# Kernel tuning notes

Hardware: AMD Instinct MI355X
Metric: run time of the kernel (lower is better)

Reference implementation:

```python
import jax, jax.numpy as jnp
import numpy as np

EPS = 1e-5


def conv1x1(x, w, b=None):
    # x: [B,C,H,W], w: [O,C] (1x1 conv kernel squeezed)
    y = jnp.einsum('bchw,oc->bohw', x, w)
    if b is not None:
        y = y + b[None, :, None, None]
    return y


def bn_inf(x, g, b, m, v):
    scale = g / jnp.sqrt(v + EPS)
    return (x - m[None, :, None, None]) * scale[None, :, None, None] + b[None, :, None, None]


def setup_inputs() -> dict:
    B, C, H, W = 2, 256, 80, 80
    Ck, Cv, Co = 64, 128, 256
    key = jax.random.key(0)
    ks = jax.random.split(key, 16)
    d = {}
    d['x'] = jax.random.normal(ks[0], (B, C, H, W), dtype=jnp.float32)
    d['y'] = jax.random.normal(ks[1], (B, C, H, W), dtype=jnp.float32)
    s = 1.0 / np.sqrt(C)
    d['fk_w'] = jax.random.normal(ks[2], (Ck, C), dtype=jnp.float32) * s
    d['fk_g'] = jnp.ones((Ck,), jnp.float32)
    d['fk_b'] = jnp.zeros((Ck,), jnp.float32)
    d['fk_m'] = jax.random.normal(ks[3], (Ck,), dtype=jnp.float32) * 0.1
    d['fk_v'] = jax.random.uniform(ks[4], (Ck,), minval=0.5, maxval=1.5, dtype=jnp.float32)
    d['fq_w'] = jax.random.normal(ks[5], (Ck, C), dtype=jnp.float32) * s
    d['fq_g'] = jnp.ones((Ck,), jnp.float32)
    d['fq_b'] = jnp.zeros((Ck,), jnp.float32)
    d['fq_m'] = jax.random.normal(ks[6], (Ck,), dtype=jnp.float32) * 0.1
    d['fq_v'] = jax.random.uniform(ks[7], (Ck,), minval=0.5, maxval=1.5, dtype=jnp.float32)
    d['fv_w'] = jax.random.normal(ks[8], (Cv, C), dtype=jnp.float32) * s
    d['fv_b'] = jnp.zeros((Cv,), jnp.float32)
    d['W_w'] = jax.random.normal(ks[9], (Co, Cv), dtype=jnp.float32) * (1.0 / np.sqrt(Cv))
    d['W_b'] = jnp.zeros((Co,), jnp.float32)
    d['gamma'] = jnp.array([0.5], jnp.float32)
    return d


def reference(x, y, fk_w, fk_g, fk_b, fk_m, fk_v, fq_w, fq_g, fq_b, fq_m, fq_v, fv_w, fv_b, W_w, W_b, gamma):
    B, C, H, W = x.shape
    Ck = fk_w.shape[0]
    Cv = fv_w.shape[0]
    N = H * W
    # key from x, query/value from y (1x1 conv + BN projections)
    k = bn_inf(conv1x1(x, fk_w), fk_g, fk_b, fk_m, fk_v).reshape(B, Ck, N)          # [B,Ck,N]
    q = bn_inf(conv1x1(y, fq_w), fq_g, fq_b, fq_m, fq_v).reshape(B, Ck, N)          # [B,Ck,N]
    v = conv1x1(y, fv_w, fv_b).reshape(B, Cv, N)                                     # [B,Cv,N]
    sim = jnp.einsum('bkn,bkm->bnm', q, k) * (Ck ** -0.5)                            # [B,N,N]
    sim = jax.nn.softmax(sim, axis=-1)
    ctx = jnp.einsum('bnm,bvm->bvn', sim, v).reshape(B, Cv, H, W)                    # [B,Cv,H,W]
    ctx = conv1x1(ctx, W_w, W_b)                                                     # [B,Co,H,W]
    return gamma[0] * ctx + x
```

## Files before the change

kernel.cpp:

```cpp
#include <hip/hip_runtime.h>
#include <math.h>

#define NB   2
#define CIN  256
#define NN   6400
#define CKd  64
#define CVd  128
#define COd  256

using bf16   = __bf16;
using bf16x4 = __attribute__((ext_vector_type(4))) bf16;
using bf16x8 = __attribute__((ext_vector_type(8))) bf16;
using f32x4  = __attribute__((ext_vector_type(4))) float;

__device__ __forceinline__ void lds_cp16(const void* g, void* l) {
    __builtin_amdgcn_global_load_lds((const __attribute__((address_space(1))) void*)g,
                                     (__attribute__((address_space(3))) void*)l, 16, 0, 0);
}

__launch_bounds__(256)
__global__ void tcvt_prep_kernel(const float* __restrict__ x, const float* __restrict__ y,
                                 bf16* __restrict__ xT, bf16* __restrict__ yT,
                                 const float* __restrict__ fk_w, const float* __restrict__ fk_g,
                                 const float* __restrict__ fk_b, const float* __restrict__ fk_m,
                                 const float* __restrict__ fk_v,
                                 const float* __restrict__ fq_w, const float* __restrict__ fq_g,
                                 const float* __restrict__ fq_b, const float* __restrict__ fq_m,
                                 const float* __restrict__ fq_v,
                                 const float* __restrict__ fv_w, const float* __restrict__ fv_b,
                                 const float* __restrict__ W_w,  const float* __restrict__ W_b,
                                 bf16* __restrict__ wkb, bf16* __restrict__ wqb,
                                 bf16* __restrict__ wvb, bf16* __restrict__ wob,
                                 float* __restrict__ bias)
{
    __shared__ __align__(16) bf16 t_lds[64][68];

    if (blockIdx.z == 4) {
        const int idx = (blockIdx.y * 100 + blockIdx.x) * 256 + threadIdx.x;
        const float QS = 0.18033688011112042f;
        if (idx < 16384) {
            const int co = idx >> 8;
            const float a = fk_g[co] * rsqrtf(fk_v[co] + 1e-5f);
            wkb[idx] = (bf16)(fk_w[idx] * a);
        } else if (idx < 32768) {
            const int i = idx - 16384, co = i >> 8;
            const float a = fq_g[co] * rsqrtf(fq_v[co] + 1e-5f) * QS;
            wqb[i] = (bf16)(fq_w[i] * a);
        } else if (idx < 65536) {
            const int i = idx - 32768;
            wvb[i] = (bf16)fv_w[i];
        } else if (idx < 98304) {
            const int i = idx - 65536;
            wob[i] = (bf16)W_w[i];
        } else if (idx < 98816) {
            const int j = idx - 98304;
            if (j < 64)       { const float a = fk_g[j] * rsqrtf(fk_v[j] + 1e-5f); bias[j] = fk_b[j] - fk_m[j] * a; }
            else if (j < 128) { const int c = j - 64; const float a = fq_g[c] * rsqrtf(fq_v[c] + 1e-5f); bias[j] = (fq_b[c] - fq_m[c] * a) * QS; }
            else if (j < 256) bias[j] = fv_b[j - 128];
            else              bias[j] = W_b[j - 256];
        }
        return;
    }

    const int b = blockIdx.z & 1;
    const float* src = (blockIdx.z >> 1) ? y : x;
    bf16* dst = (blockIdx.z >> 1) ? yT : xT;
    const int n0 = blockIdx.x * 64, c0 = blockIdx.y * 64;
    const int tid = threadIdx.x;
    const int nl = (tid & 15) * 4;
#pragma unroll
    for (int p = 0; p < 4; ++p) {
        const int cl = (tid >> 4) + p * 16;
        const float4 v = *(const float4*)(src + (size_t)(b * CIN + c0 + cl) * NN + n0 + nl);
        t_lds[nl + 0][cl] = (bf16)v.x;
        t_lds[nl + 1][cl] = (bf16)v.y;
        t_lds[nl + 2][cl] = (bf16)v.z;
        t_lds[nl + 3][cl] = (bf16)v.w;
    }
    __syncthreads();
#pragma unroll
    for (int p = 0; p < 4; ++p) {
        const int u = tid + p * 256;
        const int n = u >> 4, c4 = (u & 15) * 4;
        const bf16x4 pk = *(const bf16x4*)&t_lds[n][c4];
        *(bf16x4*)(dst + ((size_t)b * NN + n0 + n) * CIN + c0 + c4) = pk;
    }
}

__launch_bounds__(256, 2)
__global__ void projkqv_kernel(const bf16* __restrict__ xT, const bf16* __restrict__ yT,
                               const bf16* __restrict__ wkb, const bf16* __restrict__ wqb,
                               const bf16* __restrict__ wvb, const float* __restrict__ bias,
                               bf16* __restrict__ kb, bf16* __restrict__ qb, bf16* __restrict__ vb)
{
    __shared__ __align__(16) bf16 sbuf[64 * 256];
    __shared__ __align__(16) bf16 wbuf[64 * 256];

    const int tid  = threadIdx.x;
    const int lane = tid & 63, wav = tid >> 6;
    const int l15  = lane & 15, quad = lane >> 4;
    const int b    = blockIdx.z, m = blockIdx.y;
    const int n0   = blockIdx.x * 64;

    const bf16* srcg = ((m == 0) ? xT : yT) + ((size_t)b * NN + n0) * CIN;
    const bf16* wg   = (m == 0) ? wkb : (m == 1) ? wqb : (wvb + (size_t)(m - 2) * 64 * CIN);

    const int r2  = lane >> 5;
    const int c32 = lane & 31;
#pragma unroll
    for (int i = 0; i < 8; ++i) {
        const int rg = wav * 16 + i * 2;
        const int r  = rg + r2;
        const int cs = c32 ^ (r & 7);
        lds_cp16(srcg + (size_t)r * 256 + cs * 8, &sbuf[rg * 256]);
        lds_cp16(wg   + (size_t)r * 256 + cs * 8, &wbuf[rg * 256]);
    }
    __syncthreads();

    const int key = l15 & 7;
    f32x4 acc[4];
#pragma unroll
    for (int j = 0; j < 4; ++j) acc[j] = (f32x4){0.f, 0.f, 0.f, 0.f};

    if (m < 2) {
        const int arow = wav * 16 + l15;
#pragma unroll
        for (int k4 = 0; k4 < 32; k4 += 4) {
            const bf16x8 af = *(const bf16x8*)&sbuf[arow * 256 + ((k4 + quad) ^ key) * 8];
#pragma unroll
            for (int nt = 0; nt < 4; ++nt) {
                const int brow = nt * 16 + l15;
                const bf16x8 bfw = *(const bf16x8*)&wbuf[brow * 256 + ((k4 + quad) ^ key) * 8];
                acc[nt] = __builtin_amdgcn_mfma_f32_16x16x32_bf16(af, bfw, acc[nt], 0, 0, 0);
            }
        }
        const float* bs = bias + m * 64;
        bf16* dst = (m == 0) ? kb : qb;
        const int nb = n0 + wav * 16;
#pragma unroll
        for (int nt = 0; nt < 4; ++nt) {
            const float bv = bs[nt * 16 + l15];
#pragma unroll
            for (int r = 0; r < 4; ++r) {
                const int n = nb + quad * 4 + r;
                dst[((size_t)b * NN + n) * CKd + nt * 16 + l15] = (bf16)(acc[nt][r] + bv);
            }
        }
    } else {
        const int arow = wav * 16 + l15;
#pragma unroll
        for (int k4 = 0; k4 < 32; k4 += 4) {
            const bf16x8 af = *(const bf16x8*)&wbuf[arow * 256 + ((k4 + quad) ^ key) * 8];
#pragma unroll
            for (int nt = 0; nt < 4; ++nt) {
                const int brow = nt * 16 + l15;
                const bf16x8 bfy = *(const bf16x8*)&sbuf[brow * 256 + ((k4 + quad) ^ key) * 8];
                acc[nt] = __builtin_amdgcn_mfma_f32_16x16x32_bf16(af, bfy, acc[nt], 0, 0, 0);
            }
        }
        const int cv0 = (m - 2) * 64 + wav * 16;
#pragma unroll
        for (int r = 0; r < 4; ++r) {
            const int cv = cv0 + quad * 4 + r;
            const float bv = bias[128 + cv];
#pragma unroll
            for (int nt = 0; nt < 4; ++nt)
                vb[((size_t)b * CVd + cv) * NN + n0 + nt * 16 + l15] = (bf16)(acc[nt][r] + bv);
        }
    }
}

__launch_bounds__(256, 2)
__global__ void attn_kernel(const bf16* __restrict__ qb, const bf16* __restrict__ kb,
                            const bf16* __restrict__ vb,
                            bf16* __restrict__ pO, float* __restrict__ pl, int KS)
{
    __shared__ __align__(16) bf16 kbuf[2][64 * 64];
    __shared__ __align__(16) bf16 vbuf[2][128 * 64];
    __shared__ __align__(16) bf16 p_lds[4][2][16][64];

    const int lane = threadIdx.x & 63;
    const int wav  = threadIdx.x >> 6;
    const int l15  = lane & 15;
    const int quad = lane >> 4;
    const int r8   = lane >> 3;
    const int c_src = (lane & 7) ^ r8;
    const int sw   = l15 & 7;
    const int pkey = (l15 & 7) << 1;

    const int id    = blockIdx.x;
    const int ks    = id % KS;
    const int rst   = id / KS;
    const int b     = rst & 1;
    const int qtile = rst >> 1;
    const int q0    = qtile * 256 + wav * 64;

    const bf16* qrow = qb + (size_t)b * NN * CKd;
    const bf16* krow = kb + (size_t)b * NN * CKd;
    const bf16* vrow = vb + (size_t)b * CVd * NN;

    bf16x8 qf[4][2];
#pragma unroll
    for (int qt = 0; qt < 4; ++qt)
#pragma unroll
        for (int s = 0; s < 2; ++s)
            qf[qt][s] = *(const bf16x8*)(qrow + (size_t)(q0 + qt * 16 + l15) * CKd + s * 32 + quad * 8);

    f32x4 acc[4][8];
#pragma unroll
    for (int qt = 0; qt < 4; ++qt)
#pragma unroll
        for (int cv = 0; cv < 8; ++cv) acc[qt][cv] = (f32x4){0.f, 0.f, 0.f, 0.f};
    float psum[4] = {0.f, 0.f, 0.f, 0.f};

    const int t0 = (100 * ks) / KS;
    const int nt = (100 * (ks + 1)) / KS - t0;

    auto stage = [&](int t, int bi) {
        const int key0 = t * 64;
        lds_cp16(krow + (size_t)(key0 + wav * 8 + r8) * CKd + c_src * 8,
                 &kbuf[bi][(wav * 8) * 64]);
        lds_cp16(krow + (size_t)(key0 + (wav + 4) * 8 + r8) * CKd + c_src * 8,
                 &kbuf[bi][((wav + 4) * 8) * 64]);
#pragma unroll
        for (int g4 = 0; g4 < 4; ++g4) {
            const int g = wav * 4 + g4;
            lds_cp16(vrow + (size_t)(g * 8 + r8) * NN + key0 + c_src * 8,
                     &vbuf[bi][(g * 8) * 64]);
        }
    };

    stage(t0, 0);

    for (int t = 0; t < nt; ++t) {
        __syncthreads();
        if (t + 1 < nt) stage(t0 + t + 1, (t + 1) & 1);
        const bf16* kcur = &kbuf[t & 1][0];
        const bf16* vcur = &vbuf[t & 1][0];

#pragma unroll
        for (int ph = 0; ph < 2; ++ph) {
            f32x4 s4[2][4];
#pragma unroll
            for (int kt = 0; kt < 4; ++kt) {
                const int rr = kt * 16 + l15;
                const bf16x8 kf0 = *(const bf16x8*)&kcur[rr * 64 + ((quad ^ sw) * 8)];
                const bf16x8 kf1 = *(const bf16x8*)&kcur[rr * 64 + (((4 + quad) ^ sw) * 8)];
#pragma unroll
                for (int qtl = 0; qtl < 2; ++qtl) {
                    const int qt = ph * 2 + qtl;
                    f32x4 z = (f32x4){0.f, 0.f, 0.f, 0.f};
                    z = __builtin_amdgcn_mfma_f32_16x16x32_bf16(kf0, qf[qt][0], z, 0, 0, 0);
                    z = __builtin_amdgcn_mfma_f32_16x16x32_bf16(kf1, qf[qt][1], z, 0, 0, 0);
                    s4[qtl][kt] = z;
                }
            }

#pragma unroll
            for (int qtl = 0; qtl < 2; ++qtl) {
                float ps = 0.f;
#pragma unroll
                for (int kt = 0; kt < 4; ++kt) {
                    bf16x4 pk;
#pragma unroll
                    for (int r = 0; r < 4; ++r) {
                        const float p = exp2f(s4[qtl][kt][r] - 11.541560327111707f);
                        ps += p;
                        pk[r] = (bf16)p;
                    }
                    *(bf16x4*)&p_lds[wav][qtl][l15][((kt * 4 + quad) ^ pkey) * 4] = pk;
                }
                psum[ph * 2 + qtl] += ps;
            }

#pragma unroll
            for (int sp = 0; sp < 2; ++sp) {
                const bf16x8 pf0 = *(const bf16x8*)&p_lds[wav][0][l15][((sp * 8 + quad * 2) ^ pkey) * 4];
                const bf16x8 pf1 = *(const bf16x8*)&p_lds[wav][1][l15][((sp * 8 + quad * 2) ^ pkey) * 4];
#pragma unroll
                for (int cvt = 0; cvt < 8; ++cvt) {
                    const int rr = cvt * 16 + l15;
                    const bf16x8 vf = *(const bf16x8*)&vcur[rr * 64 + (((sp * 4 + quad) ^ sw) * 8)];
                    acc[ph * 2 + 0][cvt] = __builtin_amdgcn_mfma_f32_16x16x32_bf16(vf, pf0, acc[ph * 2 + 0][cvt], 0, 0, 0);
                    acc[ph * 2 + 1][cvt] = __builtin_amdgcn_mfma_f32_16x16x32_bf16(vf, pf1, acc[ph * 2 + 1][cvt], 0, 0, 0);
                }
            }
        }
    }

    __syncthreads();
    bf16* tbuf = &p_lds[wav][0][0][0];
    const size_t pb = (size_t)ks * NB + b;
#pragma unroll
    for (int qt = 0; qt < 4; ++qt) {
        psum[qt] += __shfl_xor(psum[qt], 16);
        psum[qt] += __shfl_xor(psum[qt], 32);
#pragma unroll
        for (int cvt = 0; cvt < 8; ++cvt) {
            bf16x4 pk;
#pragma unroll
            for (int r = 0; r < 4; ++r) pk[r] = (bf16)acc[qt][cvt][r];
            const int u = (cvt * 4 + quad) ^ (l15 << 1);
            *(bf16x4*)&tbuf[l15 * 128 + u * 4] = pk;
        }
#pragma unroll
        for (int j = 0; j < 4; ++j) {
            const int row = j * 4 + (lane >> 4);
            const int g   = ((lane & 15) * 2) ^ ((row & 15) << 1);
            const bf16x8 vv = *(const bf16x8*)&tbuf[row * 128 + g * 4];
            *(bf16x8*)(pO + (pb * NN + q0 + qt * 16) * CVd + j * 512 + lane * 8) = vv;
        }
        if (quad == 0) pl[pb * NN + q0 + qt * 16 + l15] = psum[qt];
    }
}

__launch_bounds__(256, 2)
__global__ void outproj_kernel(const bf16* __restrict__ pO, const float* __restrict__ pl,
                               const bf16* __restrict__ wob, const float* __restrict__ bias,
                               const float* __restrict__ x, const float* __restrict__ gam,
                               float* __restrict__ out, int KS)
{
    __shared__ __align__(16) bf16 wbuf[256 * 128];
    __shared__ __align__(16) bf16 cbuf[32 * 128];
    __shared__ float Lrow[32];

    const int tid  = threadIdx.x;
    const int lane = tid & 63, wav = tid >> 6;
    const int l15  = lane & 15, quad = lane >> 4;
    const int b    = blockIdx.y;
    const int n0   = blockIdx.x * 32;

    {
        const int r4 = lane >> 4;
        const int c  = lane & 15;
#pragma unroll
        for (int i = 0; i < 16; ++i) {
            const int rg = wav * 64 + i * 4;
            const int r  = rg + r4;
            const int cs = c ^ (r & 7);
            lds_cp16(wob + (size_t)r * CVd + cs * 8, &wbuf[rg * 128]);
        }
    }

    const int tn = tid >> 3;
    const int tc = (tid & 7) * 16;
    float vacc[16];
#pragma unroll
    for (int i = 0; i < 16; ++i) vacc[i] = 0.f;
    for (int ksi = 0; ksi < KS; ++ksi) {
        const bf16* src = pO + ((size_t)(ksi * NB + b) * NN + n0 + tn) * CVd + tc;
#pragma unroll
        for (int j = 0; j < 2; ++j) {
            const bf16x8 v = *(const bf16x8*)(src + j * 8);
#pragma unroll
            for (int e = 0; e < 8; ++e) vacc[j * 8 + e] += (float)v[e];
        }
    }
    if (tid < 32) {
        float L = 0.f;
        for (int ksi = 0; ksi < KS; ++ksi)
            L += pl[(size_t)(ksi * NB + b) * NN + n0 + tid];
        Lrow[tid] = 1.0f / L;
    }
    __syncthreads();
    {
        const float rL = Lrow[tn];
#pragma unroll
        for (int j = 0; j < 2; ++j) {
            bf16x8 o;
#pragma unroll
            for (int e = 0; e < 8; ++e) o[e] = (bf16)(vacc[j * 8 + e] * rL);
            const int c = (tid & 7) * 2 + j;
            *(bf16x8*)&cbuf[tn * 128 + ((c ^ (tn & 7)) * 8)] = o;
        }
    }
    __syncthreads();

    f32x4 acc[4][2];
#pragma unroll
    for (int i = 0; i < 4; ++i)
#pragma unroll
        for (int j = 0; j < 2; ++j) acc[i][j] = (f32x4){0.f, 0.f, 0.f, 0.f};

#pragma unroll
    for (int kk = 0; kk < 4; ++kk) {
#pragma unroll
        for (int cot = 0; cot < 4; ++cot) {
            const int arow = wav * 64 + cot * 16 + l15;
            const bf16x8 af = *(const bf16x8*)&wbuf[arow * 128 + (((kk * 4 + quad) ^ (arow & 7)) * 8)];
#pragma unroll
            for (int nt = 0; nt < 2; ++nt) {
                const int brow = nt * 16 + l15;
                const bf16x8 bfc = *(const bf16x8*)&cbuf[brow * 128 + (((kk * 4 + quad) ^ (brow & 7)) * 8)];
                acc[cot][nt] = __builtin_amdgcn_mfma_f32_16x16x32_bf16(af, bfc, acc[cot][nt], 0, 0, 0);
            }
        }
    }

    const float gm = gam[0];
#pragma unroll
    for (int cot = 0; cot < 4; ++cot) {
#pragma unroll
        for (int r = 0; r < 4; ++r) {
            const int co = wav * 64 + cot * 16 + quad * 4 + r;
            const float bv = bias[256 + co];
#pragma unroll
            for (int nt = 0; nt < 2; ++nt) {
                const int n = n0 + nt * 16 + l15;
                const size_t a = ((size_t)b * COd + co) * NN + n;
                out[a] = gm * (acc[cot][nt][r] + bv) + x[a];
            }
        }
    }
}

extern "C" void kernel_launch(void* const* d_in, const int* in_sizes, int n_in,
                              void* d_out, int out_size, void* d_ws, size_t ws_size,
                              hipStream_t stream)
{
    const float* x     = (const float*)d_in[0];
    const float* y     = (const float*)d_in[1];
    const float* fk_w  = (const float*)d_in[2];
    const float* fk_g  = (const float*)d_in[3];
    const float* fk_b  = (const float*)d_in[4];
    const float* fk_m  = (const float*)d_in[5];
    const float* fk_v  = (const float*)d_in[6];
    const float* fq_w  = (const float*)d_in[7];
    const float* fq_g  = (const float*)d_in[8];
    const float* fq_b  = (const float*)d_in[9];
    const float* fq_m  = (const float*)d_in[10];
    const float* fq_v  = (const float*)d_in[11];
    const float* fv_w  = (const float*)d_in[12];
    const float* fv_b  = (const float*)d_in[13];
    const float* W_w   = (const float*)d_in[14];
    const float* W_b   = (const float*)d_in[15];
    const float* gamma = (const float*)d_in[16];
    float* out = (float*)d_out;

    char* ws = (char*)d_ws;
    size_t off = 0;
    auto carve = [&](size_t bytes) -> char* {
        char* p = ws + off;
        off = (off + bytes + 255) & ~(size_t)255;
        return p;
    };

    bf16*  kb   = (bf16*)carve((size_t)NB * NN * CKd * 2);
    bf16*  qbuf = (bf16*)carve((size_t)NB * NN * CKd * 2);
    bf16*  vb   = (bf16*)carve((size_t)NB * CVd * NN * 2);
    bf16*  wkb  = (bf16*)carve((size_t)CKd * CIN * 2);
    bf16*  wqb  = (bf16*)carve((size_t)CKd * CIN * 2);
    bf16*  wvb  = (bf16*)carve((size_t)CVd * CIN * 2);
    bf16*  wob  = (bf16*)carve((size_t)COd * CVd * 2);
    float* bias = (float*)carve(512 * 4);

    const size_t alias_start = off;
    bf16* xT = (bf16*)carve((size_t)NB * NN * CIN * 2);
    bf16* yT = (bf16*)carve((size_t)NB * NN * CIN * 2);

    const size_t region = ws_size - alias_start;
    const size_t per_ks = (size_t)NB * NN * CVd * 2 + (size_t)NB * NN * 4 + 512;
    int KS = 1;
    {
        const int cand[6] = {10, 8, 5, 4, 2, 1};
        for (int i = 0; i < 6; ++i)
            if ((size_t)cand[i] * per_ks <= region) { KS = cand[i]; break; }
    }
    bf16*  pO = (bf16*)(ws + alias_start);
    float* pl = (float*)(ws + alias_start + (size_t)KS * NB * NN * CVd * 2);

    const dim3 blk(256);
    tcvt_prep_kernel<<<dim3(100, 4, 5), blk, 0, stream>>>(x, y, xT, yT,
                                                          fk_w, fk_g, fk_b, fk_m, fk_v,
                                                          fq_w, fq_g, fq_b, fq_m, fq_v,
                                                          fv_w, fv_b, W_w, W_b,
                                                          wkb, wqb, wvb, wob, bias);
    projkqv_kernel<<<dim3(100, 4, NB), blk, 0, stream>>>(xT, yT, wkb, wqb, wvb, bias, kb, qbuf, vb);
    attn_kernel<<<dim3(25 * NB * KS), blk, 0, stream>>>(qbuf, kb, vb, pO, pl, KS);
    outproj_kernel<<<dim3(200, NB), blk, 0, stream>>>(pO, pl, wob, bias, x, gamma, out, KS);
}
```

Before: 174.4 us.

## Fuse fp32-to-bf16 transpose of x/y into projection kernel

```diff
diff --git a/kernel.cpp b/kernel.cpp
--- a/kernel.cpp
+++ b/kernel.cpp
@@ -18,77 +18,45 @@
                                      (__attribute__((address_space(3))) void*)l, 16, 0, 0);
 }
 
-__launch_bounds__(256)
-__global__ void tcvt_prep_kernel(const float* __restrict__ x, const float* __restrict__ y,
-                                 bf16* __restrict__ xT, bf16* __restrict__ yT,
-                                 const float* __restrict__ fk_w, const float* __restrict__ fk_g,
-                                 const float* __restrict__ fk_b, const float* __restrict__ fk_m,
-                                 const float* __restrict__ fk_v,
-                                 const float* __restrict__ fq_w, const float* __restrict__ fq_g,
-                                 const float* __restrict__ fq_b, const float* __restrict__ fq_m,
-                                 const float* __restrict__ fq_v,
-                                 const float* __restrict__ fv_w, const float* __restrict__ fv_b,
-                                 const float* __restrict__ W_w,  const float* __restrict__ W_b,
-                                 bf16* __restrict__ wkb, bf16* __restrict__ wqb,
-                                 bf16* __restrict__ wvb, bf16* __restrict__ wob,
-                                 float* __restrict__ bias)
+__global__ void prep_kernel(const float* __restrict__ fk_w, const float* __restrict__ fk_g,
+                            const float* __restrict__ fk_b, const float* __restrict__ fk_m,
+                            const float* __restrict__ fk_v,
+                            const float* __restrict__ fq_w, const float* __restrict__ fq_g,
+                            const float* __restrict__ fq_b, const float* __restrict__ fq_m,
+                            const float* __restrict__ fq_v,
+                            const float* __restrict__ fv_w, const float* __restrict__ fv_b,
+                            const float* __restrict__ W_w,  const float* __restrict__ W_b,
+                            bf16* __restrict__ wkb, bf16* __restrict__ wqb,
+                            bf16* __restrict__ wvb, bf16* __restrict__ wob,
+                            float* __restrict__ bias)
 {
-    __shared__ __align__(16) bf16 t_lds[64][68];
-
-    if (blockIdx.z == 4) {
-        const int idx = (blockIdx.y * 100 + blockIdx.x) * 256 + threadIdx.x;
-        const float QS = 0.18033688011112042f;
-        if (idx < 16384) {
-            const int co = idx >> 8;
-            const float a = fk_g[co] * rsqrtf(fk_v[co] + 1e-5f);
-            wkb[idx] = (bf16)(fk_w[idx] * a);
-        } else if (idx < 32768) {
-            const int i = idx - 16384, co = i >> 8;
-            const float a = fq_g[co] * rsqrtf(fq_v[co] + 1e-5f) * QS;
-            wqb[i] = (bf16)(fq_w[i] * a);
-        } else if (idx < 65536) {
-            const int i = idx - 32768;
-            wvb[i] = (bf16)fv_w[i];
-        } else if (idx < 98304) {
-            const int i = idx - 65536;
-            wob[i] = (bf16)W_w[i];
-        } else if (idx < 98816) {
-            const int j = idx - 98304;
-            if (j < 64)       { const float a = fk_g[j] * rsqrtf(fk_v[j] + 1e-5f); bias[j] = fk_b[j] - fk_m[j] * a; }
-            else if (j < 128) { const int c = j - 64; const float a = fq_g[c] * rsqrtf(fq_v[c] + 1e-5f); bias[j] = (fq_b[c] - fq_m[c] * a) * QS; }
-            else if (j < 256) bias[j] = fv_b[j - 128];
-            else              bias[j] = W_b[j - 256];
-        }
-        return;
-    }
-
-    const int b = blockIdx.z & 1;
-    const float* src = (blockIdx.z >> 1) ? y : x;
-    bf16* dst = (blockIdx.z >> 1) ? yT : xT;
-    const int n0 = blockIdx.x * 64, c0 = blockIdx.y * 64;
-    const int tid = threadIdx.x;
-    const int nl = (tid & 15) * 4;
-#pragma unroll
-    for (int p = 0; p < 4; ++p) {
-        const int cl = (tid >> 4) + p * 16;
-        const float4 v = *(const float4*)(src + (size_t)(b * CIN + c0 + cl) * NN + n0 + nl);
-        t_lds[nl + 0][cl] = (bf16)v.x;
-        t_lds[nl + 1][cl] = (bf16)v.y;
-        t_lds[nl + 2][cl] = (bf16)v.z;
-        t_lds[nl + 3][cl] = (bf16)v.w;
-    }
-    __syncthreads();
-#pragma unroll
-    for (int p = 0; p < 4; ++p) {
-        const int u = tid + p * 256;
-        const int n = u >> 4, c4 = (u & 15) * 4;
-        const bf16x4 pk = *(const bf16x4*)&t_lds[n][c4];
-        *(bf16x4*)(dst + ((size_t)b * NN + n0 + n) * CIN + c0 + c4) = pk;
+    const int idx = blockIdx.x * 256 + threadIdx.x;
+    const float QS = 0.18033688011112042f;
+    if (idx < 16384) {
+        const int co = idx >> 8;
+        const float a = fk_g[co] * rsqrtf(fk_v[co] + 1e-5f);
+        wkb[idx] = (bf16)(fk_w[idx] * a);
+    } else if (idx < 32768) {
+        const int i = idx - 16384, co = i >> 8;
+        const float a = fq_g[co] * rsqrtf(fq_v[co] + 1e-5f) * QS;
+        wqb[i] = (bf16)(fq_w[i] * a);
+    } else if (idx < 65536) {
+        const int i = idx - 32768;
+        wvb[i] = (bf16)fv_w[i];
+    } else if (idx < 98304) {
+        const int i = idx - 65536;
+        wob[i] = (bf16)W_w[i];
+    } else if (idx < 98816) {
+        const int j = idx - 98304;
+        if (j < 64)       { const float a = fk_g[j] * rsqrtf(fk_v[j] + 1e-5f); bias[j] = fk_b[j] - fk_m[j] * a; }
+        else if (j < 128) { const int c = j - 64; const float a = fq_g[c] * rsqrtf(fq_v[c] + 1e-5f); bias[j] = (fq_b[c] - fq_m[c] * a) * QS; }
+        else if (j < 256) bias[j] = fv_b[j - 128];
+        else              bias[j] = W_b[j - 256];
     }
 }
 
 __launch_bounds__(256, 2)
-__global__ void projkqv_kernel(const bf16* __restrict__ xT, const bf16* __restrict__ yT,
+__global__ void projkqv_kernel(const float* __restrict__ x, const float* __restrict__ y,
                                const bf16* __restrict__ wkb, const bf16* __restrict__ wqb,
                                const bf16* __restrict__ wvb, const float* __restrict__ bias,
                                bf16* __restrict__ kb, bf16* __restrict__ qb, bf16* __restrict__ vb)
@@ -102,18 +70,35 @@
     const int b    = blockIdx.z, m = blockIdx.y;
     const int n0   = blockIdx.x * 64;
 
-    const bf16* srcg = ((m == 0) ? xT : yT) + ((size_t)b * NN + n0) * CIN;
-    const bf16* wg   = (m == 0) ? wkb : (m == 1) ? wqb : (wvb + (size_t)(m - 2) * 64 * CIN);
-
-    const int r2  = lane >> 5;
-    const int c32 = lane & 31;
-#pragma unroll
-    for (int i = 0; i < 8; ++i) {
-        const int rg = wav * 16 + i * 2;
-        const int r  = rg + r2;
-        const int cs = c32 ^ (r & 7);
-        lds_cp16(srcg + (size_t)r * 256 + cs * 8, &sbuf[rg * 256]);
-        lds_cp16(wg   + (size_t)r * 256 + cs * 8, &wbuf[rg * 256]);
+    const float* srcg = ((m == 0) ? x : y) + (size_t)b * CIN * NN;
+    const bf16* wg    = (m == 0) ? wkb : (m == 1) ? wqb : (wvb + (size_t)(m - 2) * 64 * CIN);
+
+    {
+        const int r2  = lane >> 5;
+        const int c32 = lane & 31;
+#pragma unroll
+        for (int i = 0; i < 8; ++i) {
+            const int rg = wav * 16 + i * 2;
+            const int r  = rg + r2;
+            const int cs = c32 ^ (r & 7);
+            lds_cp16(wg + (size_t)r * 256 + cs * 8, &wbuf[rg * 256]);
+        }
+    }
+
+    {
+        const int cb = tid >> 4;
+        const int nl = (tid & 15) * 4;
+#pragma unroll
+        for (int p = 0; p < 16; ++p) {
+            const int c = cb + p * 16;
+            const float4 v = *(const float4*)(srcg + (size_t)c * NN + n0 + nl);
+            const int c16 = c >> 3, ce = c & 7;
+#pragma unroll
+            for (int i = 0; i < 4; ++i) {
+                const int n = nl + i;
+                sbuf[n * 256 + ((c16 ^ (n & 7)) << 3) + ce] = (bf16)(&v.x)[i];
+            }
+        }
     }
     __syncthreads();
 
@@ -454,11 +439,7 @@
     bf16*  wob  = (bf16*)carve((size_t)COd * CVd * 2);
     float* bias = (float*)carve(512 * 4);
 
-    const size_t alias_start = off;
-    bf16* xT = (bf16*)carve((size_t)NB * NN * CIN * 2);
-    bf16* yT = (bf16*)carve((size_t)NB * NN * CIN * 2);
-
-    const size_t region = ws_size - alias_start;
+    const size_t region = ws_size - off;
     const size_t per_ks = (size_t)NB * NN * CVd * 2 + (size_t)NB * NN * 4 + 512;
     int KS = 1;
     {
@@ -466,16 +447,15 @@
         for (int i = 0; i < 6; ++i)
             if ((size_t)cand[i] * per_ks <= region) { KS = cand[i]; break; }
     }
-    bf16*  pO = (bf16*)(ws + alias_start);
-    float* pl = (float*)(ws + alias_start + (size_t)KS * NB * NN * CVd * 2);
+    bf16*  pO = (bf16*)carve((size_t)KS * NB * NN * CVd * 2);
+    float* pl = (float*)carve((size_t)KS * NB * NN * 4);
 
     const dim3 blk(256);
-    tcvt_prep_kernel<<<dim3(100, 4, 5), blk, 0, stream>>>(x, y, xT, yT,
-                                                          fk_w, fk_g, fk_b, fk_m, fk_v,
-                                                          fq_w, fq_g, fq_b, fq_m, fq_v,
-                                                          fv_w, fv_b, W_w, W_b,
-                                                          wkb, wqb, wvb, wob, bias);
-    projkqv_kernel<<<dim3(100, 4, NB), blk, 0, stream>>>(xT, yT, wkb, wqb, wvb, bias, kb, qbuf, vb);
+    prep_kernel<<<386, blk, 0, stream>>>(fk_w, fk_g, fk_b, fk_m, fk_v,
+                                         fq_w, fq_g, fq_b, fq_m, fq_v,
+                                         fv_w, fv_b, W_w, W_b,
+                                         wkb, wqb, wvb, wob, bias);
+    projkqv_kernel<<<dim3(100, 4, NB), blk, 0, stream>>>(x, y, wkb, wqb, wvb, bias, kb, qbuf, vb);
     attn_kernel<<<dim3(25 * NB * KS), blk, 0, stream>>>(qbuf, kb, vb, pO, pl, KS);
     outproj_kernel<<<dim3(200, NB), blk, 0, stream>>>(pO, pl, wob, bias, x, gamma, out, KS);
 }
```

Result: no change. 173.7 us (-0.4%).
